# Kernel optimization log

Measured on AMD Instinct MI355X. Metric: run time of the kernel, lower is better.

The kernel has to match this reference:

```python
import jax, jax.numpy as jnp
import numpy as np

N_NODES = 100000
N_EDGES = 1600000
IN_F = 128
OUT_F = 32


def setup_inputs() -> dict:
    key = jax.random.key(0)
    k1, k2, k3 = jax.random.split(key, 3)
    x = jax.random.normal(k1, (N_NODES, IN_F), dtype=jnp.float32)
    edge_index = jax.random.randint(k2, (2, N_EDGES), 0, N_NODES, dtype=jnp.int64)
    W = jax.random.normal(k3, (OUT_F, IN_F), dtype=jnp.float32) * 0.1
    b = jnp.zeros((OUT_F,), dtype=jnp.float32)
    return {"x": x, "edge_index": edge_index, "W": W, "b": b}


def reference(x, edge_index, W, b):
    # PyG GCNConv: add self-loops, symmetric normalization, linear, aggregate, bias
    N = x.shape[0]
    loops = jnp.arange(N, dtype=edge_index.dtype)
    src = jnp.concatenate([edge_index[0], loops])  # message source j
    dst = jnp.concatenate([edge_index[1], loops])  # aggregation target i
    ones = jnp.ones(src.shape[0], dtype=x.dtype)
    deg = jax.ops.segment_sum(ones, dst, num_segments=N)  # deg computed at col (target)
    dis = jnp.where(deg > 0, jax.lax.rsqrt(deg), 0.0)  # deg^{-1/2}, inf -> 0
    norm = dis[src] * dis[dst]  # [E+N]
    h = x @ W.T  # [N, OUT_F] linear transform first (PyG order)
    msg = h[src] * norm[:, None]  # [E+N, OUT_F] gathered, normalized messages
    out = jax.ops.segment_sum(msg, dst, num_segments=N)  # scatter-add aggregate
    return out + b
```

## Files before the change

### kernel.cpp

```cpp
#include <hip/hip_runtime.h>

#define IN_F 128
#define OUT_F 32
#define BKT_SHIFT 9
#define BKT_NODES 512
#define NBKT 196
#define PART_CHUNK 4096
#define SORT_CAP 12288
#define GEMM_NPB 128

typedef unsigned int uint32;
typedef __attribute__((ext_vector_type(8))) short bf16x8;
typedef __attribute__((ext_vector_type(4))) float f32x4;

__device__ __forceinline__ float bf2f(uint32 u) {
    union { uint32 ui; float f; } c; c.ui = u << 16; return c.f;
}
__device__ __forceinline__ uint32 f2bf(float x) {
    union { float f; uint32 ui; } c; c.f = x;
    uint32 u = c.ui;
    u += 0x7fffu + ((u >> 16) & 1u);
    return u >> 16;
}
__device__ __forceinline__ bf16x8 pack8(float4 lo, float4 hi) {
    union { bf16x8 v; uint32 u[4]; } r;
    r.u[0] = f2bf(lo.x) | (f2bf(lo.y) << 16);
    r.u[1] = f2bf(lo.z) | (f2bf(lo.w) << 16);
    r.u[2] = f2bf(hi.x) | (f2bf(hi.y) << 16);
    r.u[3] = f2bf(hi.z) | (f2bf(hi.w) << 16);
    return r.v;
}

__global__ void __launch_bounds__(512) k_phist(const int* __restrict__ dst,
        int* __restrict__ T, int E, int EB) {
    __shared__ int h8[8][256];
    int t = threadIdx.x;
    int wv = t >> 6;
    for (int i = t; i < 8 * 256; i += 512) ((int*)h8)[i] = 0;
    __syncthreads();
    int base = blockIdx.x * PART_CHUNK;
    #pragma unroll
    for (int i = 0; i < 8; ++i) {
        int e = base + i * 512 + t;
        if (e < E) atomicAdd(&h8[wv][dst[e] >> BKT_SHIFT], 1);
    }
    __syncthreads();
    if (t < NBKT) {
        int s = 0;
        #pragma unroll
        for (int w = 0; w < 8; ++w) s += h8[w][t];
        T[t * EB + blockIdx.x] = s;
    }
}

__global__ void __launch_bounds__(256) k_oscan_a(
        int* __restrict__ T, int* __restrict__ partials, int M) {
    __shared__ int sc[256];
    int t = threadIdx.x;
    int base = blockIdx.x * 512;
    int i0 = base + 2 * t, i1 = i0 + 1;
    int d0 = (i0 < M) ? T[i0] : 0;
    int d1 = (i1 < M) ? T[i1] : 0;
    sc[t] = d0 + d1;
    __syncthreads();
    #pragma unroll
    for (int ofs = 1; ofs < 256; ofs <<= 1) {
        int v = sc[t];
        int u = (t >= ofs) ? sc[t - ofs] : 0;
        __syncthreads();
        sc[t] = v + u;
        __syncthreads();
    }
    int eT = t ? sc[t - 1] : 0;
    if (i0 < M) T[i0] = eT;
    if (i1 < M) T[i1] = eT + d0;
    if (t == 0) partials[blockIdx.x] = sc[255];
}

__global__ void __launch_bounds__(256) k_oscan_b(
        const int* __restrict__ partials, int* __restrict__ bases, int nb) {
    __shared__ int sc[256];
    int t = threadIdx.x;
    sc[t] = (t < nb) ? partials[t] : 0;
    __syncthreads();
    #pragma unroll
    for (int ofs = 1; ofs < 256; ofs <<= 1) {
        int v = sc[t];
        int u = (t >= ofs) ? sc[t - ofs] : 0;
        __syncthreads();
        sc[t] = v + u;
        __syncthreads();
    }
    bases[t] = t ? sc[t - 1] : 0;
}

__global__ void __launch_bounds__(512) k_part(
        const int* __restrict__ src, const int* __restrict__ dst,
        const int* __restrict__ T, const int* __restrict__ obases,
        uint32* __restrict__ pk, int E, int EB) {
    __shared__ int    h8[8][256];
    __shared__ int    hTot[256];
    __shared__ int    sc[256];
    __shared__ int    cbase[256];
    __shared__ int    gbase[256];
    __shared__ uint32 stage[PART_CHUNK];
    int t = threadIdx.x;
    int wv = t >> 6;
    for (int i = t; i < 8 * 256; i += 512) ((int*)h8)[i] = 0;
    __syncthreads();
    int base = blockIdx.x * PART_CHUNK;

    int bkt[8], rank[8];
    uint32 val[8];
    #pragma unroll
    for (int i = 0; i < 8; ++i) {
        int e = base + i * 512 + t;
        if (e < E) {
            int d = dst[e];
            int s = src[e];
            int b = d >> BKT_SHIFT;
            bkt[i] = b;
            val[i] = (uint32)s | ((uint32)(d & (BKT_NODES - 1)) << 17);
            rank[i] = atomicAdd(&h8[wv][b], 1);
        } else {
            bkt[i] = -1;
        }
    }
    __syncthreads();
    if (t < 256) {
        int run = 0;
        #pragma unroll
        for (int w = 0; w < 8; ++w) {
            int tmp = h8[w][t];
            h8[w][t] = run;
            run += tmp;
        }
        hTot[t] = run;
        sc[t] = run;
    }
    __syncthreads();
    #pragma unroll
    for (int ofs = 1; ofs < 256; ofs <<= 1) {
        int v = 0, u = 0;
        if (t < 256) { v = sc[t]; u = (t >= ofs) ? sc[t - ofs] : 0; }
        __syncthreads();
        if (t < 256) sc[t] = v + u;
        __syncthreads();
    }
    if (t < 256) cbase[t] = t ? sc[t - 1] : 0;
    if (t < NBKT) {
        int idx = t * EB + blockIdx.x;
        gbase[t] = T[idx] + obases[idx >> 9];
    }
    __syncthreads();
    #pragma unroll
    for (int i = 0; i < 8; ++i)
        if (bkt[i] >= 0) stage[cbase[bkt[i]] + h8[wv][bkt[i]] + rank[i]] = val[i];
    __syncthreads();
    int wave = t >> 6, lane = t & 63;
    for (int b = wave; b < NBKT; b += 8) {
        int cnt_b = hTot[b];
        int cb = cbase[b], gb = gbase[b];
        for (int s = lane; s < cnt_b; s += 64)
            pk[gb + s] = stage[cb + s];
    }
}

__global__ void __launch_bounds__(512) k_sg(
        uint32* __restrict__ pk, const int* __restrict__ T,
        const int* __restrict__ obases, int* __restrict__ cursor,
        float* __restrict__ dis,
        const float* __restrict__ x, const float* __restrict__ W,
        unsigned short* __restrict__ gbf, int n, int E, int EB) {
    if (blockIdx.x < NBKT) {
        __shared__ uint32 stg[SORT_CAP];
        __shared__ int    cnt[BKT_NODES];
        __shared__ int    sc[256];
        int b = blockIdx.x, t = threadIdx.x;
        int nodeBase = b * BKT_NODES;
        int i0 = b * EB;
        int start = T[i0] + obases[i0 >> 9];
        int end;
        if (b + 1 < NBKT) {
            int i1 = (b + 1) * EB;
            end = T[i1] + obases[i1 >> 9];
        } else {
            end = E;
        }
        int len = end - start;
        if (t < BKT_NODES) cnt[t] = 0;
        __syncthreads();
        for (int i = t; i < len; i += 512) atomicAdd(&cnt[pk[start + i] >> 17], 1);
        __syncthreads();
        int c0 = 0, c1 = 0;
        if (t < 256) { c0 = cnt[2 * t]; c1 = cnt[2 * t + 1]; sc[t] = c0 + c1; }
        __syncthreads();
        #pragma unroll
        for (int ofs = 1; ofs < 256; ofs <<= 1) {
            int v = 0, u = 0;
            if (t < 256) { v = sc[t]; u = (t >= ofs) ? sc[t - ofs] : 0; }
            __syncthreads();
            if (t < 256) sc[t] = v + u;
            __syncthreads();
        }
        if (t < 256) {
            int eT = t ? sc[t - 1] : 0;
            cnt[2 * t]     = eT;
            cnt[2 * t + 1] = eT + c0;
            int n0 = nodeBase + 2 * t;
            if (n0 < n) {
                cursor[n0] = start + eT;
                dis[n0] = rsqrtf((float)(c0 + 1));
                int n1 = n0 + 1;
                if (n1 < n) {
                    cursor[n1] = start + eT + c0;
                    dis[n1] = rsqrtf((float)(c1 + 1));
                }
            }
        }
        __syncthreads();
        for (int i = t; i < len; i += 512) {
            uint32 p = pk[start + i];
            int pos = atomicAdd(&cnt[p >> 17], 1);
            stg[pos] = p & 0x1FFFFu;
        }
        __syncthreads();
        for (int i = t; i < len; i += 512) pk[start + i] = stg[i];
    } else {
        int gid = blockIdx.x - NBKT;
        int lane = threadIdx.x & 63;
        int wv   = threadIdx.x >> 6;
        int nodeBase = gid * GEMM_NPB + wv * 16;
        int r16 = lane & 15;
        int kg  = lane >> 4;
        int arow = nodeBase + r16;
        if (arow >= n) arow = n - 1;
        const float4* xr = (const float4*)(x + (size_t)arow * IN_F);
        bf16x8 afr[4];
        #pragma unroll
        for (int kk = 0; kk < 4; ++kk) {
            int c4 = kk * 8 + kg * 2;
            afr[kk] = pack8(xr[c4], xr[c4 + 1]);
        }
        bf16x8 bfr[2][4];
        #pragma unroll
        for (int fb = 0; fb < 2; ++fb) {
            const float4* wr = (const float4*)(W + (size_t)(fb * 16 + r16) * IN_F);
            #pragma unroll
            for (int kk = 0; kk < 4; ++kk) {
                int c4 = kk * 8 + kg * 2;
                bfr[fb][kk] = pack8(wr[c4], wr[c4 + 1]);
            }
        }
        f32x4 acc0 = {0.f, 0.f, 0.f, 0.f};
        f32x4 acc1 = {0.f, 0.f, 0.f, 0.f};
        #pragma unroll
        for (int kk = 0; kk < 4; ++kk) {
            acc0 = __builtin_amdgcn_mfma_f32_16x16x32_bf16(afr[kk], bfr[0][kk], acc0, 0, 0, 0);
            acc1 = __builtin_amdgcn_mfma_f32_16x16x32_bf16(afr[kk], bfr[1][kk], acc1, 0, 0, 0);
        }
        #pragma unroll
        for (int j = 0; j < 4; ++j) {
            int node = nodeBase + kg * 4 + j;
            if (node < n) {
                gbf[node * OUT_F + r16]      = (unsigned short)f2bf(acc0[j]);
                gbf[node * OUT_F + 16 + r16] = (unsigned short)f2bf(acc1[j]);
            }
        }
    }
}

__global__ void __launch_bounds__(256) k_aggr(
        const uint32* __restrict__ g2, const uint32* __restrict__ pk,
        const int* __restrict__ cursor, const float* __restrict__ dis,
        const float* __restrict__ b, float* __restrict__ out, int n, int E) {
    int tid = threadIdx.x;
    int node = blockIdx.x * 32 + (tid >> 3);
    if (node >= n) return;
    int l = tid & 7;
    const uint2* g2v = (const uint2*)g2;
    int start = cursor[node];
    int end   = (node + 1 < n) ? cursor[node + 1] : E;
    float dd = dis[node];
    uint2 vs = g2v[node * 8 + l];
    float a0 = bf2f(vs.x & 0xffffu) * dd;
    float a1 = bf2f(vs.x >> 16) * dd;
    float a2 = bf2f(vs.y & 0xffffu) * dd;
    float a3 = bf2f(vs.y >> 16) * dd;
    float c0 = 0.f, c1 = 0.f, c2 = 0.f, c3 = 0.f;
    int e = start;
    for (; e + 4 <= end; e += 4) {
        int s0 = pk[e], s1 = pk[e + 1], s2 = pk[e + 2], s3 = pk[e + 3];
        uint2 v0 = g2v[s0 * 8 + l];
        uint2 v1 = g2v[s1 * 8 + l];
        uint2 v2 = g2v[s2 * 8 + l];
        uint2 v3 = g2v[s3 * 8 + l];
        float w0 = dis[s0], w1 = dis[s1], w2 = dis[s2], w3 = dis[s3];
        a0 += bf2f(v0.x & 0xffffu) * w0; a1 += bf2f(v0.x >> 16) * w0;
        a2 += bf2f(v0.y & 0xffffu) * w0; a3 += bf2f(v0.y >> 16) * w0;
        c0 += bf2f(v1.x & 0xffffu) * w1; c1 += bf2f(v1.x >> 16) * w1;
        c2 += bf2f(v1.y & 0xffffu) * w1; c3 += bf2f(v1.y >> 16) * w1;
        a0 += bf2f(v2.x & 0xffffu) * w2; a1 += bf2f(v2.x >> 16) * w2;
        a2 += bf2f(v2.y & 0xffffu) * w2; a3 += bf2f(v2.y >> 16) * w2;
        c0 += bf2f(v3.x & 0xffffu) * w3; c1 += bf2f(v3.x >> 16) * w3;
        c2 += bf2f(v3.y & 0xffffu) * w3; c3 += bf2f(v3.y >> 16) * w3;
    }
    for (; e < end; ++e) {
        int s = pk[e];
        uint2 v = g2v[s * 8 + l];
        float w = dis[s];
        a0 += bf2f(v.x & 0xffffu) * w; a1 += bf2f(v.x >> 16) * w;
        a2 += bf2f(v.y & 0xffffu) * w; a3 += bf2f(v.y >> 16) * w;
    }
    float4 bb = ((const float4*)b)[l];
    float4 o;
    o.x = dd * (a0 + c0) + bb.x;
    o.y = dd * (a1 + c1) + bb.y;
    o.z = dd * (a2 + c2) + bb.z;
    o.w = dd * (a3 + c3) + bb.w;
    ((float4*)out)[node * 8 + l] = o;
}

extern "C" void kernel_launch(void* const* d_in, const int* in_sizes, int n_in,
                              void* d_out, int out_size, void* d_ws, size_t ws_size,
                              hipStream_t stream) {
    const float* x  = (const float*)d_in[0];
    const int*   ei = (const int*)d_in[1];
    const float* W  = (const float*)d_in[2];
    const float* b  = (const float*)d_in[3];
    float* out = (float*)d_out;

    int N = in_sizes[0] / IN_F;
    int E = in_sizes[1] / 2;
    const int* src = ei;
    const int* dst = ei + E;

    int EB = (E + PART_CHUNK - 1) / PART_CHUNK;
    int M  = NBKT * EB;

    char* p = (char*)d_ws;
    int*            T        = (int*)p;            p += ((size_t)M * 4 + 255) & ~255ull;
    int*            partials = (int*)p;            p += 2048;
    int*            obases   = (int*)p;            p += 2048;
    int*            cursor   = (int*)p;            p += ((size_t)N * 4 + 255) & ~255ull;
    float*          dis      = (float*)p;          p += ((size_t)N * 4 + 255) & ~255ull;
    uint32*         pkbuf    = (uint32*)p;         p += ((size_t)E * 4 + 255) & ~255ull;
    unsigned short* gbf      = (unsigned short*)p; p += ((size_t)N * OUT_F * 2 + 255) & ~255ull;

    int nsb = (M + 511) / 512;
    int gemmBlocks = (N + GEMM_NPB - 1) / GEMM_NPB;

    k_phist<<<EB, 512, 0, stream>>>(dst, T, E, EB);
    k_oscan_a<<<nsb, 256, 0, stream>>>(T, partials, M);
    k_oscan_b<<<1, 256, 0, stream>>>(partials, obases, nsb);
    k_part<<<EB, 512, 0, stream>>>(src, dst, T, obases, pkbuf, E, EB);
    k_sg<<<NBKT + gemmBlocks, 512, 0, stream>>>(
        pkbuf, T, obases, cursor, dis, x, W, gbf, N, E, EB);
    k_aggr<<<(N + 31) / 32, 256, 0, stream>>>(
        (const uint32*)gbf, pkbuf, cursor, dis, b, out, N, E);
}
```

Measured before the change: 159.6 us.

## Fuse bucket sort with aggregation via cooperative grid sync; move GEMM into histogram kernel

The GEMM blocks move from the sort kernel into the histogram kernel so the linear transform overlaps the partition histogram. The per-bucket counting sort and the aggregation are merged into one cooperative kernel with 1024 threads per bucket. Sorted source ids stay in LDS across a grid-wide sync, which removes the write-back of sorted edges, the cursor array and a separate kernel launch. The partition scatter now precomputes target indices so the global write is a flat loop. In exchange, only 196 blocks with 1024 threads do the aggregation, which limits parallelism in the gather, and the cooperative launch adds a grid barrier.

Result: slower. 239.4 us (+50.0%).

```diff
diff --git a/kernel.cpp b/kernel.cpp
--- a/kernel.cpp
+++ b/kernel.cpp
@@ -1,4 +1,7 @@
 #include <hip/hip_runtime.h>
+#include <hip/hip_cooperative_groups.h>
+
+namespace cg = cooperative_groups;
 
 #define IN_F 128
 #define OUT_F 32
@@ -31,25 +34,70 @@
     return r.v;
 }
 
-__global__ void __launch_bounds__(512) k_phist(const int* __restrict__ dst,
-        int* __restrict__ T, int E, int EB) {
-    __shared__ int h8[8][256];
-    int t = threadIdx.x;
-    int wv = t >> 6;
-    for (int i = t; i < 8 * 256; i += 512) ((int*)h8)[i] = 0;
-    __syncthreads();
-    int base = blockIdx.x * PART_CHUNK;
-    #pragma unroll
-    for (int i = 0; i < 8; ++i) {
-        int e = base + i * 512 + t;
-        if (e < E) atomicAdd(&h8[wv][dst[e] >> BKT_SHIFT], 1);
-    }
-    __syncthreads();
-    if (t < NBKT) {
-        int s = 0;
-        #pragma unroll
-        for (int w = 0; w < 8; ++w) s += h8[w][t];
-        T[t * EB + blockIdx.x] = s;
+__global__ void __launch_bounds__(512) k_pg(
+        const int* __restrict__ dst, int* __restrict__ T,
+        const float* __restrict__ x, const float* __restrict__ W,
+        unsigned short* __restrict__ gbf, int n, int E, int EB) {
+    if ((int)blockIdx.x < EB) {
+        __shared__ int h8[8][256];
+        int t = threadIdx.x;
+        int wv = t >> 6;
+        for (int i = t; i < 8 * 256; i += 512) ((int*)h8)[i] = 0;
+        __syncthreads();
+        int base = blockIdx.x * PART_CHUNK;
+        #pragma unroll
+        for (int i = 0; i < 8; ++i) {
+            int e = base + i * 512 + t;
+            if (e < E) atomicAdd(&h8[wv][dst[e] >> BKT_SHIFT], 1);
+        }
+        __syncthreads();
+        if (t < NBKT) {
+            int s = 0;
+            #pragma unroll
+            for (int w = 0; w < 8; ++w) s += h8[w][t];
+            T[t * EB + blockIdx.x] = s;
+        }
+    } else {
+        int gid = blockIdx.x - EB;
+        int lane = threadIdx.x & 63;
+        int wv   = threadIdx.x >> 6;
+        int nodeBase = gid * GEMM_NPB + wv * 16;
+        int r16 = lane & 15;
+        int kg  = lane >> 4;
+        int arow = nodeBase + r16;
+        if (arow >= n) arow = n - 1;
+        const float4* xr = (const float4*)(x + (size_t)arow * IN_F);
+        bf16x8 afr[4];
+        #pragma unroll
+        for (int kk = 0; kk < 4; ++kk) {
+            int c4 = kk * 8 + kg * 2;
+            afr[kk] = pack8(xr[c4], xr[c4 + 1]);
+        }
+        bf16x8 bfr[2][4];
+        #pragma unroll
+        for (int fb = 0; fb < 2; ++fb) {
+            const float4* wr = (const float4*)(W + (size_t)(fb * 16 + r16) * IN_F);
+            #pragma unroll
+            for (int kk = 0; kk < 4; ++kk) {
+                int c4 = kk * 8 + kg * 2;
+                bfr[fb][kk] = pack8(wr[c4], wr[c4 + 1]);
+            }
+        }
+        f32x4 acc0 = {0.f, 0.f, 0.f, 0.f};
+        f32x4 acc1 = {0.f, 0.f, 0.f, 0.f};
+        #pragma unroll
+        for (int kk = 0; kk < 4; ++kk) {
+            acc0 = __builtin_amdgcn_mfma_f32_16x16x32_bf16(afr[kk], bfr[0][kk], acc0, 0, 0, 0);
+            acc1 = __builtin_amdgcn_mfma_f32_16x16x32_bf16(afr[kk], bfr[1][kk], acc1, 0, 0, 0);
+        }
+        #pragma unroll
+        for (int j = 0; j < 4; ++j) {
+            int node = nodeBase + kg * 4 + j;
+            if (node < n) {
+                gbf[node * OUT_F + r16]      = (unsigned short)f2bf(acc0[j]);
+                gbf[node * OUT_F + 16 + r16] = (unsigned short)f2bf(acc1[j]);
+            }
+        }
     }
 }
 
@@ -104,11 +152,13 @@
     __shared__ int    cbase[256];
     __shared__ int    gbase[256];
     __shared__ uint32 stage[PART_CHUNK];
+    __shared__ int    tgtb[PART_CHUNK];
     int t = threadIdx.x;
     int wv = t >> 6;
     for (int i = t; i < 8 * 256; i += 512) ((int*)h8)[i] = 0;
     __syncthreads();
     int base = blockIdx.x * PART_CHUNK;
+    int lenChunk = E - base; if (lenChunk > PART_CHUNK) lenChunk = PART_CHUNK;
 
     int bkt[8], rank[8];
     uint32 val[8];
@@ -154,171 +204,123 @@
     }
     __syncthreads();
     #pragma unroll
-    for (int i = 0; i < 8; ++i)
-        if (bkt[i] >= 0) stage[cbase[bkt[i]] + h8[wv][bkt[i]] + rank[i]] = val[i];
-    __syncthreads();
-    int wave = t >> 6, lane = t & 63;
-    for (int b = wave; b < NBKT; b += 8) {
-        int cnt_b = hTot[b];
-        int cb = cbase[b], gb = gbase[b];
-        for (int s = lane; s < cnt_b; s += 64)
-            pk[gb + s] = stage[cb + s];
-    }
-}
-
-__global__ void __launch_bounds__(512) k_sg(
-        uint32* __restrict__ pk, const int* __restrict__ T,
-        const int* __restrict__ obases, int* __restrict__ cursor,
-        float* __restrict__ dis,
-        const float* __restrict__ x, const float* __restrict__ W,
-        unsigned short* __restrict__ gbf, int n, int E, int EB) {
-    if (blockIdx.x < NBKT) {
-        __shared__ uint32 stg[SORT_CAP];
-        __shared__ int    cnt[BKT_NODES];
-        __shared__ int    sc[256];
-        int b = blockIdx.x, t = threadIdx.x;
-        int nodeBase = b * BKT_NODES;
-        int i0 = b * EB;
-        int start = T[i0] + obases[i0 >> 9];
-        int end;
-        if (b + 1 < NBKT) {
-            int i1 = (b + 1) * EB;
-            end = T[i1] + obases[i1 >> 9];
-        } else {
-            end = E;
-        }
-        int len = end - start;
-        if (t < BKT_NODES) cnt[t] = 0;
-        __syncthreads();
-        for (int i = t; i < len; i += 512) atomicAdd(&cnt[pk[start + i] >> 17], 1);
-        __syncthreads();
-        int c0 = 0, c1 = 0;
-        if (t < 256) { c0 = cnt[2 * t]; c1 = cnt[2 * t + 1]; sc[t] = c0 + c1; }
-        __syncthreads();
-        #pragma unroll
-        for (int ofs = 1; ofs < 256; ofs <<= 1) {
-            int v = 0, u = 0;
-            if (t < 256) { v = sc[t]; u = (t >= ofs) ? sc[t - ofs] : 0; }
-            __syncthreads();
-            if (t < 256) sc[t] = v + u;
-            __syncthreads();
-        }
-        if (t < 256) {
-            int eT = t ? sc[t - 1] : 0;
-            cnt[2 * t]     = eT;
-            cnt[2 * t + 1] = eT + c0;
-            int n0 = nodeBase + 2 * t;
-            if (n0 < n) {
-                cursor[n0] = start + eT;
-                dis[n0] = rsqrtf((float)(c0 + 1));
-                int n1 = n0 + 1;
-                if (n1 < n) {
-                    cursor[n1] = start + eT + c0;
-                    dis[n1] = rsqrtf((float)(c1 + 1));
-                }
-            }
-        }
-        __syncthreads();
-        for (int i = t; i < len; i += 512) {
-            uint32 p = pk[start + i];
-            int pos = atomicAdd(&cnt[p >> 17], 1);
-            stg[pos] = p & 0x1FFFFu;
-        }
-        __syncthreads();
-        for (int i = t; i < len; i += 512) pk[start + i] = stg[i];
+    for (int i = 0; i < 8; ++i) {
+        if (bkt[i] >= 0) {
+            int b = bkt[i];
+            int loc = h8[wv][b] + rank[i];
+            int cpos = cbase[b] + loc;
+            stage[cpos] = val[i];
+            tgtb[cpos]  = gbase[b] + loc;
+        }
+    }
+    __syncthreads();
+    for (int i = t; i < lenChunk; i += 512) pk[tgtb[i]] = stage[i];
+}
+
+__global__ void __launch_bounds__(1024) k_sa(
+        const uint32* __restrict__ pk, const int* __restrict__ T,
+        const int* __restrict__ obases, float* __restrict__ dis,
+        const unsigned short* __restrict__ gbf, const float* __restrict__ bias,
+        float* __restrict__ out, int n, int E, int EB) {
+    __shared__ uint32 stg[SORT_CAP];
+    __shared__ int    cnt[BKT_NODES];
+    __shared__ int    cstart[BKT_NODES];
+    __shared__ int    sc[256];
+    int b = blockIdx.x, t = threadIdx.x;
+    int nodeBase = b * BKT_NODES;
+    int i0 = b * EB;
+    int start = T[i0] + obases[i0 >> 9];
+    int end;
+    if (b + 1 < (int)gridDim.x) {
+        int i1 = (b + 1) * EB;
+        end = T[i1] + obases[i1 >> 9];
     } else {
-        int gid = blockIdx.x - NBKT;
-        int lane = threadIdx.x & 63;
-        int wv   = threadIdx.x >> 6;
-        int nodeBase = gid * GEMM_NPB + wv * 16;
-        int r16 = lane & 15;
-        int kg  = lane >> 4;
-        int arow = nodeBase + r16;
-        if (arow >= n) arow = n - 1;
-        const float4* xr = (const float4*)(x + (size_t)arow * IN_F);
-        bf16x8 afr[4];
-        #pragma unroll
-        for (int kk = 0; kk < 4; ++kk) {
-            int c4 = kk * 8 + kg * 2;
-            afr[kk] = pack8(xr[c4], xr[c4 + 1]);
-        }
-        bf16x8 bfr[2][4];
-        #pragma unroll
-        for (int fb = 0; fb < 2; ++fb) {
-            const float4* wr = (const float4*)(W + (size_t)(fb * 16 + r16) * IN_F);
-            #pragma unroll
-            for (int kk = 0; kk < 4; ++kk) {
-                int c4 = kk * 8 + kg * 2;
-                bfr[fb][kk] = pack8(wr[c4], wr[c4 + 1]);
-            }
-        }
-        f32x4 acc0 = {0.f, 0.f, 0.f, 0.f};
-        f32x4 acc1 = {0.f, 0.f, 0.f, 0.f};
-        #pragma unroll
-        for (int kk = 0; kk < 4; ++kk) {
-            acc0 = __builtin_amdgcn_mfma_f32_16x16x32_bf16(afr[kk], bfr[0][kk], acc0, 0, 0, 0);
-            acc1 = __builtin_amdgcn_mfma_f32_16x16x32_bf16(afr[kk], bfr[1][kk], acc1, 0, 0, 0);
-        }
-        #pragma unroll
-        for (int j = 0; j < 4; ++j) {
-            int node = nodeBase + kg * 4 + j;
-            if (node < n) {
-                gbf[node * OUT_F + r16]      = (unsigned short)f2bf(acc0[j]);
-                gbf[node * OUT_F + 16 + r16] = (unsigned short)f2bf(acc1[j]);
-            }
-        }
-    }
-}
-
-__global__ void __launch_bounds__(256) k_aggr(
-        const uint32* __restrict__ g2, const uint32* __restrict__ pk,
-        const int* __restrict__ cursor, const float* __restrict__ dis,
-        const float* __restrict__ b, float* __restrict__ out, int n, int E) {
-    int tid = threadIdx.x;
-    int node = blockIdx.x * 32 + (tid >> 3);
-    if (node >= n) return;
-    int l = tid & 7;
-    const uint2* g2v = (const uint2*)g2;
-    int start = cursor[node];
-    int end   = (node + 1 < n) ? cursor[node + 1] : E;
-    float dd = dis[node];
-    uint2 vs = g2v[node * 8 + l];
-    float a0 = bf2f(vs.x & 0xffffu) * dd;
-    float a1 = bf2f(vs.x >> 16) * dd;
-    float a2 = bf2f(vs.y & 0xffffu) * dd;
-    float a3 = bf2f(vs.y >> 16) * dd;
-    float c0 = 0.f, c1 = 0.f, c2 = 0.f, c3 = 0.f;
-    int e = start;
-    for (; e + 4 <= end; e += 4) {
-        int s0 = pk[e], s1 = pk[e + 1], s2 = pk[e + 2], s3 = pk[e + 3];
-        uint2 v0 = g2v[s0 * 8 + l];
-        uint2 v1 = g2v[s1 * 8 + l];
-        uint2 v2 = g2v[s2 * 8 + l];
-        uint2 v3 = g2v[s3 * 8 + l];
-        float w0 = dis[s0], w1 = dis[s1], w2 = dis[s2], w3 = dis[s3];
-        a0 += bf2f(v0.x & 0xffffu) * w0; a1 += bf2f(v0.x >> 16) * w0;
-        a2 += bf2f(v0.y & 0xffffu) * w0; a3 += bf2f(v0.y >> 16) * w0;
-        c0 += bf2f(v1.x & 0xffffu) * w1; c1 += bf2f(v1.x >> 16) * w1;
-        c2 += bf2f(v1.y & 0xffffu) * w1; c3 += bf2f(v1.y >> 16) * w1;
-        a0 += bf2f(v2.x & 0xffffu) * w2; a1 += bf2f(v2.x >> 16) * w2;
-        a2 += bf2f(v2.y & 0xffffu) * w2; a3 += bf2f(v2.y >> 16) * w2;
-        c0 += bf2f(v3.x & 0xffffu) * w3; c1 += bf2f(v3.x >> 16) * w3;
-        c2 += bf2f(v3.y & 0xffffu) * w3; c3 += bf2f(v3.y >> 16) * w3;
-    }
-    for (; e < end; ++e) {
-        int s = pk[e];
-        uint2 v = g2v[s * 8 + l];
-        float w = dis[s];
-        a0 += bf2f(v.x & 0xffffu) * w; a1 += bf2f(v.x >> 16) * w;
-        a2 += bf2f(v.y & 0xffffu) * w; a3 += bf2f(v.y >> 16) * w;
-    }
-    float4 bb = ((const float4*)b)[l];
-    float4 o;
-    o.x = dd * (a0 + c0) + bb.x;
-    o.y = dd * (a1 + c1) + bb.y;
-    o.z = dd * (a2 + c2) + bb.z;
-    o.w = dd * (a3 + c3) + bb.w;
-    ((float4*)out)[node * 8 + l] = o;
+        end = E;
+    }
+    int len = end - start;
+    if (t < BKT_NODES) cnt[t] = 0;
+    __syncthreads();
+    for (int i = t; i < len; i += 1024) atomicAdd(&cnt[pk[start + i] >> 17], 1);
+    __syncthreads();
+    int c0 = 0, c1 = 0;
+    if (t < 256) { c0 = cnt[2 * t]; c1 = cnt[2 * t + 1]; sc[t] = c0 + c1; }
+    __syncthreads();
+    #pragma unroll
+    for (int ofs = 1; ofs < 256; ofs <<= 1) {
+        int v = 0, u = 0;
+        if (t < 256) { v = sc[t]; u = (t >= ofs) ? sc[t - ofs] : 0; }
+        __syncthreads();
+        if (t < 256) sc[t] = v + u;
+        __syncthreads();
+    }
+    if (t < 256) {
+        int eT = t ? sc[t - 1] : 0;
+        cstart[2 * t]     = eT;
+        cstart[2 * t + 1] = eT + c0;
+        cnt[2 * t]     = eT;
+        cnt[2 * t + 1] = eT + c0;
+        int n0 = nodeBase + 2 * t;
+        if (n0 < n) {
+            dis[n0] = rsqrtf((float)(c0 + 1));
+            int n1 = n0 + 1;
+            if (n1 < n) dis[n1] = rsqrtf((float)(c1 + 1));
+        }
+    }
+    __syncthreads();
+    for (int i = t; i < len; i += 1024) {
+        uint32 p = pk[start + i];
+        int pos = atomicAdd(&cnt[p >> 17], 1);
+        stg[pos] = p & 0x1FFFFu;
+    }
+    __threadfence();
+    cg::this_grid().sync();
+    const uint2* g2v = (const uint2*)gbf;
+    int l = t & 7, slot = t >> 3;
+    float4 bb = ((const float4*)bias)[l];
+    for (int nb2 = 0; nb2 < BKT_NODES; nb2 += 128) {
+        int nl = nb2 + slot;
+        int node = nodeBase + nl;
+        if (node >= n) continue;
+        int s  = cstart[nl];
+        int en = cnt[nl];
+        float dd = rsqrtf((float)(en - s + 1));
+        uint2 vs = g2v[(size_t)node * 8 + l];
+        float a0 = bf2f(vs.x & 0xffffu) * dd;
+        float a1 = bf2f(vs.x >> 16) * dd;
+        float a2 = bf2f(vs.y & 0xffffu) * dd;
+        float a3 = bf2f(vs.y >> 16) * dd;
+        float q0 = 0.f, q1 = 0.f, q2 = 0.f, q3 = 0.f;
+        int e = s;
+        for (; e + 4 <= en; e += 4) {
+            int s0 = stg[e], s1 = stg[e + 1], s2 = stg[e + 2], s3 = stg[e + 3];
+            uint2 v0 = g2v[s0 * 8 + l];
+            uint2 v1 = g2v[s1 * 8 + l];
+            uint2 v2 = g2v[s2 * 8 + l];
+            uint2 v3 = g2v[s3 * 8 + l];
+            float w0 = dis[s0], w1 = dis[s1], w2 = dis[s2], w3 = dis[s3];
+            a0 += bf2f(v0.x & 0xffffu) * w0; a1 += bf2f(v0.x >> 16) * w0;
+            a2 += bf2f(v0.y & 0xffffu) * w0; a3 += bf2f(v0.y >> 16) * w0;
+            q0 += bf2f(v1.x & 0xffffu) * w1; q1 += bf2f(v1.x >> 16) * w1;
+            q2 += bf2f(v1.y & 0xffffu) * w1; q3 += bf2f(v1.y >> 16) * w1;
+            a0 += bf2f(v2.x & 0xffffu) * w2; a1 += bf2f(v2.x >> 16) * w2;
+            a2 += bf2f(v2.y & 0xffffu) * w2; a3 += bf2f(v2.y >> 16) * w2;
+            q0 += bf2f(v3.x & 0xffffu) * w3; q1 += bf2f(v3.x >> 16) * w3;
+            q2 += bf2f(v3.y & 0xffffu) * w3; q3 += bf2f(v3.y >> 16) * w3;
+        }
+        for (; e < en; ++e) {
+            int sid = stg[e];
+            uint2 v = g2v[sid * 8 + l];
+            float w = dis[sid];
+            a0 += bf2f(v.x & 0xffffu) * w; a1 += bf2f(v.x >> 16) * w;
+            a2 += bf2f(v.y & 0xffffu) * w; a3 += bf2f(v.y >> 16) * w;
+        }
+        float4 o;
+        o.x = dd * (a0 + q0) + bb.x;
+        o.y = dd * (a1 + q1) + bb.y;
+        o.z = dd * (a2 + q2) + bb.z;
+        o.w = dd * (a3 + q3) + bb.w;
+        ((float4*)out)[(size_t)node * 8 + l] = o;
+    }
 }
 
 extern "C" void kernel_launch(void* const* d_in, const int* in_sizes, int n_in,
@@ -342,20 +344,26 @@
     int*            T        = (int*)p;            p += ((size_t)M * 4 + 255) & ~255ull;
     int*            partials = (int*)p;            p += 2048;
     int*            obases   = (int*)p;            p += 2048;
-    int*            cursor   = (int*)p;            p += ((size_t)N * 4 + 255) & ~255ull;
     float*          dis      = (float*)p;          p += ((size_t)N * 4 + 255) & ~255ull;
     uint32*         pkbuf    = (uint32*)p;         p += ((size_t)E * 4 + 255) & ~255ull;
     unsigned short* gbf      = (unsigned short*)p; p += ((size_t)N * OUT_F * 2 + 255) & ~255ull;
 
     int nsb = (M + 511) / 512;
     int gemmBlocks = (N + GEMM_NPB - 1) / GEMM_NPB;
-
-    k_phist<<<EB, 512, 0, stream>>>(dst, T, E, EB);
+    int nbkt = (N + BKT_NODES - 1) / BKT_NODES;
+
+    k_pg<<<EB + gemmBlocks, 512, 0, stream>>>(dst, T, x, W, gbf, N, E, EB);
     k_oscan_a<<<nsb, 256, 0, stream>>>(T, partials, M);
     k_oscan_b<<<1, 256, 0, stream>>>(partials, obases, nsb);
     k_part<<<EB, 512, 0, stream>>>(src, dst, T, obases, pkbuf, E, EB);
-    k_sg<<<NBKT + gemmBlocks, 512, 0, stream>>>(
-        pkbuf, T, obases, cursor, dis, x, W, gbf, N, E, EB);
-    k_aggr<<<(N + 31) / 32, 256, 0, stream>>>(
-        (const uint32*)gbf, pkbuf, cursor, dis, b, out, N, E);
-}
+
+    const uint32* pk_c = pkbuf;
+    const int* T_c = T;
+    const int* ob_c = obases;
+    const unsigned short* gbf_c = gbf;
+    const float* b_c = b;
+    void* args[] = { (void*)&pk_c, (void*)&T_c, (void*)&ob_c, (void*)&dis,
+                     (void*)&gbf_c, (void*)&b_c, (void*)&out,
+                     (void*)&N, (void*)&E, (void*)&EB };
+    hipLaunchCooperativeKernel((void*)k_sa, dim3(nbkt), dim3(1024), args, 0, stream);
+}
```
